# Optimization experiments

Measured on AMD Instinct MI355X. Metric: run time of the kernel, lower is better.

The kernel has to match this reference:

```python
import jax, jax.numpy as jnp
import numpy as np

DT = 0.001
TAU_SYN_INV = 200.0  # norse default 1/5e-3
TAU_MEM_INV = 100.0  # norse default 1/1e-2
V_TH = 0.4
ALPHA = 10.0  # SuperSpike surrogate slope


@jax.custom_vjp
def heaviside(x):
    # SuperSpike: heaviside forward, 1/(alpha*|x|+1)^2 surrogate backward
    return (x > 0).astype(x.dtype)

def _h_fwd(x):
    return heaviside(x), x

def _h_bwd(x, g):
    return (g / (ALPHA * jnp.abs(x) + 1.0) ** 2,)

heaviside.defvjp(_h_fwd, _h_bwd)


def conv(x, w, b, stride=1):
    y = jax.lax.conv_general_dilated(
        x, w, (stride, stride), 'VALID',
        dimension_numbers=('NCHW', 'OIHW', 'NCHW'))
    return y + b[None, :, None, None]


def maxpool2(x):
    return jax.lax.reduce_window(x, -jnp.inf, jax.lax.max, (1, 1, 2, 2), (1, 1, 2, 2), 'VALID')


def setup_inputs() -> dict:
    key = jax.random.key(0)
    ks = jax.random.split(key, 11)
    B, T, H, W = 32, 64, 64, 64
    num_classes = 10
    F = 96 * 12 * 12  # flattened encoder size = 13824
    HID = 128

    def u(k, shape, fan_in):
        bound = 1.0 / np.sqrt(fan_in)
        return jax.random.uniform(k, shape, jnp.float32, -bound, bound)

    return dict(
        x=jax.random.normal(ks[0], (B, T, 1, H, W), jnp.float32),
        w1=u(ks[1], (32, 1, 5, 5), 25), b1=u(ks[2], (32,), 25),
        w2=u(ks[3], (64, 32, 3, 3), 32 * 9), b2=u(ks[4], (64,), 32 * 9),
        w3=u(ks[5], (96, 64, 3, 3), 64 * 9), b3=u(ks[6], (96,), 64 * 9),
        w_in=jax.random.normal(ks[7], (HID, F), jnp.float32) / np.sqrt(F),
        w_rec=jax.random.normal(ks[8], (HID, HID), jnp.float32) / np.sqrt(HID),
        w_fc=u(ks[9], (num_classes, HID), HID),
        b_fc=u(ks[10], (num_classes,), HID),
    )


def reference(x, w1, b1, w2, b2, w3, b3, w_in, w_rec, w_fc, b_fc):
    B, T = x.shape[0], x.shape[1]
    HID = w_in.shape[0]
    C = w_fc.shape[0]

    # encoder vectorized over all B*T frames
    frames = x.reshape(B * T, x.shape[2], x.shape[3], x.shape[4])
    z = jax.nn.relu(conv(frames, w1, b1, stride=2))  # [BT,32,30,30]
    z = jax.nn.relu(conv(z, w2, b2))                 # [BT,64,28,28]
    z = maxpool2(z)                                  # [BT,64,14,14]
    z = jax.nn.relu(conv(z, w3, b3))                 # [BT,96,12,12]
    feats = z.reshape(B, T, -1)                      # [B,T,13824]

    # precompute feed-forward input currents for all timesteps
    ff = jnp.einsum('btf,hf->tbh', feats, w_in)      # [T,B,HID]

    def step(carry, ff_t):
        z_p, v, i, vr, ir = carry
        # LIF recurrent cell (norse lif_step, v_leak=0, v_reset=0)
        v_dec = v + DT * TAU_MEM_INV * (-v + i)
        i_dec = i - DT * TAU_SYN_INV * i
        z_n = heaviside(v_dec - V_TH)
        v_n = (1.0 - z_n) * v_dec
        i_n = i_dec + ff_t + z_p @ w_rec.T  # recurrent uses previous spikes
        # readout linear + LI cell (norse li_feed_forward_step)
        ro = z_n @ w_fc.T + b_fc
        vr_n = vr + DT * TAU_MEM_INV * (-vr + ir)
        ir_n = ir - DT * TAU_SYN_INV * ir + ro
        return (z_n, v_n, i_n, vr_n, ir_n), vr_n

    zeros_h = jnp.zeros((B, HID), x.dtype)
    zeros_c = jnp.zeros((B, C), x.dtype)
    carry0 = (zeros_h, zeros_h, zeros_h, zeros_c, zeros_c)
    _, voltages = jax.lax.scan(step, carry0, ff)     # [T,B,C]

    out = jnp.max(voltages, axis=0)                  # [B,C]
    return jax.nn.log_softmax(out, axis=1)
```

## Files before the change

### kernel.cpp

```cpp
#include <hip/hip_runtime.h>
#include <math.h>

typedef _Float16 half8 __attribute__((ext_vector_type(8)));
typedef _Float16 half4 __attribute__((ext_vector_type(4)));
typedef float f32x16 __attribute__((ext_vector_type(16)));

__global__ __launch_bounds__(256) void xprep_k(const float* __restrict__ x,
                                               _Float16* __restrict__ xh,
                                               _Float16* __restrict__ xl) {
  const int i = blockIdx.x * 256 + threadIdx.x;
  if (i >= 2097152) return;
  const float4 v = *(const float4*)(x + (size_t)i * 4);
  half4 h, l;
  const float vv[4] = {v.x, v.y, v.z, v.w};
#pragma unroll
  for (int e = 0; e < 4; ++e) {
    const _Float16 hh = (_Float16)vv[e];
    h[e] = hh;
    l[e] = (_Float16)((vv[e] - (float)hh) * 1024.0f);
  }
  *(half4*)(xh + (size_t)i * 4) = h;
  *(half4*)(xl + (size_t)i * 4) = l;
}

__global__ __launch_bounds__(256) void w1prep_k(const float* __restrict__ w1,
                                                _Float16* __restrict__ w1p) {
  const int i = blockIdx.x * 256 + threadIdx.x;
  if (i >= 1024) return;
  const int blk = i >> 8;
  const int s = blk >> 1, g = blk & 1;
  const int ch = (i >> 3) & 31, e = i & 7;
  const int k = s * 16 + g * 8 + e;
  float v = 0.f;
  if (k < 25) v = w1[ch * 25 + k];
  const _Float16 h = (_Float16)v;
  w1p[i] = h;
  w1p[1024 + i] = (_Float16)((v - (float)h) * 1024.0f);
}

__global__ __launch_bounds__(256) void w2prep_k(const float* __restrict__ w2,
                                                _Float16* __restrict__ w2p) {
  const int i = blockIdx.x * 256 + threadIdx.x;
  if (i >= 18432) return;
  const int tap = i >> 11;
  const int r = i & 2047;
  const int blk = r >> 8;
  const int nt = blk >> 2, s = (blk >> 1) & 1, g = blk & 1;
  const int n = (r >> 3) & 31, e = r & 7;
  const int och = nt * 32 + n;
  const int ic = s * 16 + g * 8 + e;
  const float v = w2[och * 288 + ic * 9 + tap];
  const _Float16 h = (_Float16)v;
  const _Float16 l = (_Float16)((v - (float)h) * 1024.0f);
  w2p[i] = h;
  w2p[18432 + i] = l;
}

__global__ __launch_bounds__(256) void w3prep_k(const float* __restrict__ w3,
                                                _Float16* __restrict__ w3p) {
  const int i = blockIdx.x * 256 + threadIdx.x;
  if (i >= 55296) return;
  const int icc = i / 27648;
  const int r1 = i - icc * 27648;
  const int tc = r1 / 6144;
  const int rem = r1 - tc * 6144;
  const int tl = rem / 3072;
  const int rem2 = rem - tl * 3072;
  const int nt = rem2 >> 10;
  const int s = (rem2 >> 9) & 1;
  const int g = (rem2 >> 8) & 1;
  const int n = (rem2 >> 3) & 31;
  const int e = rem2 & 7;
  const int tap = tc * 2 + tl;
  const int och = nt * 32 + n;
  const int ic = icc * 32 + s * 16 + g * 8 + e;
  const float v = w3[(size_t)och * 576 + ic * 9 + tap];
  const _Float16 h = (_Float16)v;
  const _Float16 l = (_Float16)((v - (float)h) * 1024.0f);
  w3p[i] = h;
  w3p[55296 + i] = l;
}

__global__ __launch_bounds__(256) void winprep_k(const float* __restrict__ w_in,
                                                 _Float16* __restrict__ winp) {
  const int i = blockIdx.x * 256 + threadIdx.x;
  if (i >= 1769472) return;
  const int ks = i >> 11;
  const int rem = i & 2047;
  const int nt = rem >> 9;
  const int g = (rem >> 8) & 1;
  const int n = (rem >> 3) & 31;
  const int e = rem & 7;
  const int h = nt * 32 + n;
  const int k = ks * 16 + g * 8 + e;
  const float v = w_in[(size_t)h * 13824 + k];
  const _Float16 hh = (_Float16)v;
  const _Float16 ll = (_Float16)((v - (float)hh) * 1024.0f);
  winp[i] = hh;
  winp[1769472 + i] = ll;
}

__global__ __launch_bounds__(448) void conv2f_mfma_k(
    const _Float16* __restrict__ xh, const _Float16* __restrict__ xl,
    const float* __restrict__ b1, const _Float16* __restrict__ w1p,
    const _Float16* __restrict__ w2p, const float* __restrict__ b2,
    _Float16* __restrict__ y2s) {
  __shared__ __align__(16) _Float16 S[31232];
  const int rp = blockIdx.x;
  const int img0 = blockIdx.y * 2;
  const int tid = threadIdx.x;

  const int w = tid >> 6;
  const int lane = tid & 63;
  const int l31 = lane & 31;
  const int g = lane >> 5;

  {
    const float b1c = b1[l31];
    const int gb = l31 >> 3, e0 = l31 & 7;
    int xoffs[16];
#pragma unroll
    for (int s = 0; s < 2; ++s)
#pragma unroll
      for (int e = 0; e < 8; ++e) {
        const int k = s * 16 + g * 8 + e;
        const int ky = k / 5, kx = k - (k / 5) * 5;
        xoffs[s * 8 + e] = (k < 25) ? (ky * 64 + kx) : -1;
      }
#pragma unroll 1
    for (int ph = 0; ph < 2; ++ph) {
      if (tid < 240) {
        const int plane = tid / 120;
        const int c8 = tid - plane * 120;
        const _Float16* src = (plane ? xl : xh) +
                              (size_t)(img0 + ph) * 4096 + rp * 512 + c8 * 8;
        *(float4*)&S[23040 + plane * 960 + c8 * 8] = *(const float4*)src;
      }
      __syncthreads();
      if (w < 6) {
        const int p = w * 32 + l31;
        const int pcl = (p < 180) ? p : 179;
        const int row = pcl / 30;
        const int col = pcl - row * 30;
        const int xb = (2 * row) * 64 + 2 * col;
        f32x16 acc_h = {}, acc_l = {};
#pragma unroll
        for (int s = 0; s < 2; ++s) {
          half8 ah, al;
#pragma unroll
          for (int e = 0; e < 8; ++e) {
            const int o = xoffs[s * 8 + e];
            _Float16 hv = (_Float16)0.f, lv = (_Float16)0.f;
            if (o >= 0) {
              hv = S[23040 + xb + o];
              lv = S[24000 + xb + o];
            }
            ah[e] = hv;
            al[e] = lv;
          }
          const _Float16* bp = w1p + ((s * 2 + g) * 32 + l31) * 8;
          half8 bh = *(const half8*)bp;
          half8 bl = *(const half8*)(bp + 1024);
          acc_h = __builtin_amdgcn_mfma_f32_32x32x16_f16(ah, bh, acc_h, 0, 0, 0);
          acc_l = __builtin_amdgcn_mfma_f32_32x32x16_f16(ah, bl, acc_l, 0, 0, 0);
          acc_l = __builtin_amdgcn_mfma_f32_32x32x16_f16(al, bh, acc_l, 0, 0, 0);
        }
#pragma unroll
        for (int r = 0; r < 16; ++r) {
          const int mrow = (r & 3) + 8 * (r >> 2) + 4 * g;
          const int pp = w * 32 + mrow;
          if (pp < 180) {
            const int cl = pp - (pp / 30) * 30;
            const int swz = (cl >> 1) & 3;
            const int addr = ph * 5760 + pp * 32 + ((gb ^ swz) << 3) + e0;
            const float val =
                fmaxf(acc_h[r] + acc_l[r] * 9.765625e-4f + b1c, 0.f);
            const _Float16 hh = (_Float16)val;
            S[addr] = hh;
            S[11520 + addr] = (_Float16)((val - (float)hh) * 1024.0f);
          }
        }
      }
      __syncthreads();
    }
  }

  const int m = w * 32 + l31;
  const int aimg = m / 112;
  const int apos = m - aimg * 112;
  const int ar = apos / 28;
  const int ax = apos - ar * 28;
  const int icg = g * 8;

  f32x16 acc00 = {}, acc01 = {}, acc10 = {}, acc11 = {};

#pragma unroll 1
  for (int tc = 0; tc < 5; ++tc) {
    __syncthreads();
    const int tap0 = tc * 2;
    const int ntaps = (tc == 4) ? 1 : 2;
    for (int c = tid; c < ntaps * 256; c += 448) {
      *(float4*)&S[23040 + c * 8] = *(const float4*)&w2p[tap0 * 2048 + c * 8];
      *(float4*)&S[27136 + c * 8] =
          *(const float4*)&w2p[18432 + tap0 * 2048 + c * 8];
    }
    __syncthreads();
#pragma unroll 1
    for (int tl = 0; tl < ntaps; ++tl) {
      const int tap = tap0 + tl;
      const int ky = tap / 3;
      const int kx = tap - ky * 3;
      const int acol = ax + kx;
      const int swzA = ((acol >> 1) & 3) << 3;
      const int abase = aimg * 5760 + ((ar + ky) * 30 + acol) * 32;
#pragma unroll
      for (int s = 0; s < 2; ++s) {
        const int icoA = (s * 16 + icg) ^ swzA;
        const int bo0 = 23040 + (((tl * 2 + 0) * 2 + s) * 2 + g) * 256 + l31 * 8;
        const int bo1 = 23040 + (((tl * 2 + 1) * 2 + s) * 2 + g) * 256 + l31 * 8;
        half8 ah = *(const half8*)&S[abase + icoA];
        half8 al = *(const half8*)&S[11520 + abase + icoA];
        half8 bh0 = *(const half8*)&S[bo0];
        half8 bl0 = *(const half8*)&S[bo0 + 4096];
        half8 bh1 = *(const half8*)&S[bo1];
        half8 bl1 = *(const half8*)&S[bo1 + 4096];
        acc00 = __builtin_amdgcn_mfma_f32_32x32x16_f16(ah, bh0, acc00, 0, 0, 0);
        acc10 = __builtin_amdgcn_mfma_f32_32x32x16_f16(ah, bl0, acc10, 0, 0, 0);
        acc10 = __builtin_amdgcn_mfma_f32_32x32x16_f16(al, bh0, acc10, 0, 0, 0);
        acc01 = __builtin_amdgcn_mfma_f32_32x32x16_f16(ah, bh1, acc01, 0, 0, 0);
        acc11 = __builtin_amdgcn_mfma_f32_32x32x16_f16(ah, bl1, acc11, 0, 0, 0);
        acc11 = __builtin_amdgcn_mfma_f32_32x32x16_f16(al, bh1, acc11, 0, 0, 0);
      }
    }
  }

  float* sPool = (float*)S;
#pragma unroll 1
  for (int ph = 0; ph < 2; ++ph) {
    __syncthreads();
#pragma unroll
    for (int r = 0; r < 16; ++r) {
      const int mrow = (r & 3) + 8 * (r >> 2) + 4 * g;
      const int mo = w * 32 + mrow;
      const int srow = mo - ph * 112;
      if (srow >= 0 && srow < 112) {
        sPool[srow * 68 + l31] = acc00[r] + acc10[r] * 9.765625e-4f;
        sPool[srow * 68 + 32 + l31] = acc01[r] + acc11[r] * 9.765625e-4f;
      }
    }
    __syncthreads();
    if (tid < 224) {
      const int pr = tid / 112;
      const int r2 = tid - pr * 112;
      const int pc = r2 >> 3;
      const int blk = r2 & 7;
      const int m00 = pr * 56 + pc * 2;
      const float* s0 = &sPool[m00 * 68 + blk * 8];
      float rowv[4][8];
      *(float4*)&rowv[0][0] = *(const float4*)s0;
      *(float4*)&rowv[0][4] = *(const float4*)(s0 + 4);
      *(float4*)&rowv[1][0] = *(const float4*)(s0 + 68);
      *(float4*)&rowv[1][4] = *(const float4*)(s0 + 72);
      *(float4*)&rowv[2][0] = *(const float4*)(s0 + 28 * 68);
      *(float4*)&rowv[2][4] = *(const float4*)(s0 + 28 * 68 + 4);
      *(float4*)&rowv[3][0] = *(const float4*)(s0 + 29 * 68);
      *(float4*)&rowv[3][4] = *(const float4*)(s0 + 29 * 68 + 4);
      half8 hv, lv;
#pragma unroll
      for (int e = 0; e < 8; ++e) {
        const float mx = fmaxf(fmaxf(rowv[0][e], rowv[1][e]),
                               fmaxf(rowv[2][e], rowv[3][e]));
        const float val = fmaxf(mx + b2[blk * 8 + e], 0.f);
        const _Float16 hh = (_Float16)val;
        hv[e] = hh;
        lv[e] = (_Float16)((val - (float)hh) * 1024.0f);
      }
      const int posg = (rp * 2 + pr) * 14 + pc;
      const int icc = blk >> 2;
      const int slot = (blk & 3) ^ ((posg >> 1) & 3);
      _Float16* dh = y2s + (size_t)(img0 + ph) * 25088 + icc * 6272 +
                     posg * 32 + slot * 8;
      *(float4*)dh = *(float4*)&hv;
      *(float4*)(dh + 12544) = *(float4*)&lv;
    }
  }
}

__global__ __launch_bounds__(320) void conv3_mfma_k(
    const _Float16* __restrict__ y2s, const _Float16* __restrict__ w3p,
    const float* __restrict__ b3, _Float16* __restrict__ fh,
    _Float16* __restrict__ fl) {
  __shared__ __align__(16) _Float16 S[12544];
  const int img = blockIdx.x;
  const int tid = threadIdx.x;
  const int w = tid >> 6;
  const int lane = tid & 63;
  const int l31 = lane & 31;
  const int g = lane >> 5;
  const int m = w * 32 + l31;
  const int mc = (m < 144) ? m : 143;
  const int r = mc / 12, c = mc - (mc / 12) * 12;

  f32x16 acch[3] = {};
  f32x16 accl[3] = {};

  const _Float16* bb = w3p + g * 256 + l31 * 8;
#pragma unroll 1
  for (int icc = 0; icc < 2; ++icc) {
    __syncthreads();
    {
      const _Float16* src = y2s + (size_t)img * 25088 + icc * 6272;
      for (int c8 = tid; c8 < 784; c8 += 320) {
        *(float4*)&S[c8 * 8] = *(const float4*)&src[c8 * 8];
        *(float4*)&S[6272 + c8 * 8] = *(const float4*)&src[12544 + c8 * 8];
      }
    }
    __syncthreads();
#pragma unroll 1
    for (int tc = 0; tc < 5; ++tc) {
      const int ntaps = (tc == 4) ? 1 : 2;
#pragma unroll 1
      for (int tl = 0; tl < ntaps; ++tl) {
        const int tap = tc * 2 + tl;
        const int ky = tap / 3, kx = tap - (tap / 3) * 3;
        const int pix = (r + ky) * 14 + (c + kx);
        const int pswz = (pix >> 1) & 3;
        half8 ah[2], al[2];
#pragma unroll
        for (int s = 0; s < 2; ++s) {
          const int o = pix * 32 + ((s * 2 + g) ^ pswz) * 8;
          ah[s] = *(const half8*)&S[o];
          al[s] = *(const half8*)&S[6272 + o];
        }
        const _Float16* bt = bb + icc * 27648 + tc * 6144 + tl * 3072;
#pragma unroll
        for (int nt = 0; nt < 3; ++nt) {
#pragma unroll
          for (int s = 0; s < 2; ++s) {
            const _Float16* bp = bt + nt * 1024 + s * 512;
            half8 bh = *(const half8*)bp;
            half8 bl = *(const half8*)(bp + 55296);
            acch[nt] =
                __builtin_amdgcn_mfma_f32_32x32x16_f16(ah[s], bh, acch[nt], 0, 0, 0);
            accl[nt] =
                __builtin_amdgcn_mfma_f32_32x32x16_f16(ah[s], bl, accl[nt], 0, 0, 0);
            accl[nt] =
                __builtin_amdgcn_mfma_f32_32x32x16_f16(al[s], bh, accl[nt], 0, 0, 0);
          }
        }
      }
    }
  }
  float* sO = (float*)S;
#pragma unroll
  for (int nt = 0; nt < 3; ++nt) {
    __syncthreads();
#pragma unroll
    for (int rr = 0; rr < 16; ++rr) {
      const int row = (rr & 3) + 8 * (rr >> 2) + 4 * g;
      const int pos = w * 32 + row;
      if (pos < 144)
        sO[l31 * 145 + pos] = acch[nt][rr] + accl[nt][rr] * 9.765625e-4f;
    }
    __syncthreads();
    for (int idx8 = tid; idx8 < 576; idx8 += 320) {
      const int oc = idx8 / 18;
      const int pb = idx8 - oc * 18;
      const float bb2 = b3[nt * 32 + oc];
      half8 hv, lv;
#pragma unroll
      for (int e = 0; e < 8; ++e) {
        const float v = fmaxf(sO[oc * 145 + pb * 8 + e] + bb2, 0.f);
        const _Float16 hh = (_Float16)v;
        hv[e] = hh;
        lv[e] = (_Float16)((v - (float)hh) * 1024.0f);
      }
      const size_t ko = (size_t)img * 13824 + (nt * 32 + oc) * 144 + pb * 8;
      *(float4*)&fh[ko] = *(float4*)&hv;
      *(float4*)&fl[ko] = *(float4*)&lv;
    }
  }
}

__global__ __launch_bounds__(256) void ffgemm_k(
    const _Float16* __restrict__ fh, const _Float16* __restrict__ fl,
    const _Float16* __restrict__ winp, float* __restrict__ P, int frame0,
    int Cl) {
  __shared__ __align__(16) _Float16 S[24576];
  const int mb = blockIdx.x;
  const int kc = blockIdx.y;
  const int tid = threadIdx.x;
  const int w = tid >> 6;
  const int lane = tid & 63;
  const int l31 = lane & 31;
  const int g = lane >> 5;
  const int mt = w >> 1;
  const int nt0 = (w & 1) * 2;
  f32x16 acc_h[2] = {};
  f32x16 acc_l[2] = {};
  const int kbase = kc * 1728;
#pragma unroll 1
  for (int kt = 0; kt < 27; ++kt) {
    __syncthreads();
    for (int i = tid; i < 512; i += 256) {
      const int row = i >> 3, kb = i & 7;
      int rc = mb * 64 + row;
      if (rc >= Cl) rc = Cl - 1;
      const size_t so = (size_t)rc * 13824 + kbase + kt * 64 + kb * 8;
      const int d = row * 64 + ((kb ^ (row & 7)) * 8);
      *(float4*)&S[d] = *(const float4*)&fh[so];
      *(float4*)&S[4096 + d] = *(const float4*)&fl[so];
    }
    {
      const size_t bo = (size_t)(kc * 108 + kt * 4) * 2048;
      for (int i = tid; i < 1024; i += 256) {
        *(float4*)&S[8192 + i * 8] = *(const float4*)&winp[bo + i * 8];
        *(float4*)&S[16384 + i * 8] =
            *(const float4*)&winp[1769472 + bo + i * 8];
      }
    }
    __syncthreads();
#pragma unroll
    for (int ks = 0; ks < 4; ++ks) {
      const int kb = ks * 2 + g;
      const int ao = (mt * 32 + l31) * 64 + ((kb ^ (l31 & 7)) * 8);
      half8 ah = *(const half8*)&S[ao];
      half8 al = *(const half8*)&S[4096 + ao];
#pragma unroll
      for (int j = 0; j < 2; ++j) {
        const int nt = nt0 + j;
        const int b = 8192 + (((ks * 4 + nt) * 2 + g) * 32 + l31) * 8;
        half8 bh = *(const half8*)&S[b];
        half8 bl = *(const half8*)&S[8192 + b];
        acc_h[j] = __builtin_amdgcn_mfma_f32_32x32x16_f16(ah, bh, acc_h[j], 0, 0, 0);
        acc_l[j] = __builtin_amdgcn_mfma_f32_32x32x16_f16(ah, bl, acc_l[j], 0, 0, 0);
        acc_l[j] = __builtin_amdgcn_mfma_f32_32x32x16_f16(al, bh, acc_l[j], 0, 0, 0);
      }
    }
  }
  float* Pp = P + ((size_t)kc * 2048 + (size_t)frame0) * 128;
#pragma unroll
  for (int j = 0; j < 2; ++j) {
    const int h = (nt0 + j) * 32 + l31;
#pragma unroll
    for (int r = 0; r < 16; ++r) {
      const int row = (r & 3) + 8 * (r >> 2) + 4 * g;
      const int fr = mb * 64 + mt * 32 + row;
      if (fr < Cl)
        Pp[(size_t)fr * 128 + h] = acc_h[j][r] + acc_l[j][r] * 9.765625e-4f;
    }
  }
}

__global__ __launch_bounds__(256) void ffreduce_k(const float* __restrict__ P,
                                                  float* __restrict__ ffo) {
  const int i = blockIdx.x * 256 + threadIdx.x;
  float s = 0.f;
#pragma unroll
  for (int kcc = 0; kcc < 8; ++kcc) s += P[(size_t)kcc * 262144 + i];
  ffo[i] = s;
}

__global__ __launch_bounds__(64) void scan_k(
    const float* __restrict__ ff, const float* __restrict__ w_rec,
    const float* __restrict__ w_fc, const float* __restrict__ b_fc,
    float* __restrict__ out) {
#pragma clang fp contract(off)
  __shared__ float sWr[16384];
  const int b = blockIdx.x;
  const int t = threadIdx.x;
  for (int idx = t; idx < 16384; idx += 64) {
    int hh = idx >> 7, j = idx & 127;
    sWr[j * 128 + hh] = w_rec[idx];
  }
  float wf0[10], wf1[10], bf[10];
#pragma unroll
  for (int c = 0; c < 10; ++c) {
    wf0[c] = w_fc[c * 128 + t];
    wf1[c] = w_fc[c * 128 + 64 + t];
    bf[c] = b_fc[c];
  }
  __syncthreads();
  float v0 = 0.f, v1 = 0.f, i0 = 0.f, i1 = 0.f;
  float vr[10], ir[10], vmax[10];
#pragma unroll
  for (int c = 0; c < 10; ++c) {
    vr[c] = 0.f;
    ir[c] = 0.f;
    vmax[c] = -1e30f;
  }
  unsigned long long pm0 = 0ull, pm1 = 0ull;
  const float* ffb = ff + (size_t)b * 8192;
#pragma unroll 1
  for (int ts = 0; ts < 64; ++ts) {
    const float vd0 = v0 + 0.1f * (i0 - v0);
    const float vd1 = v1 + 0.1f * (i1 - v1);
    const float id0 = i0 - 0.2f * i0;
    const float id1 = i1 - 0.2f * i1;
    const bool z0 = (vd0 - 0.4f) > 0.f;
    const bool z1 = (vd1 - 0.4f) > 0.f;
    v0 = z0 ? 0.f : vd0;
    v1 = z1 ? 0.f : vd1;
    float rec0 = 0.f, rec1 = 0.f;
    unsigned long long mm = pm0;
    while (mm) {
      int j = __ffsll(mm) - 1;
      mm &= mm - 1;
      rec0 += sWr[j * 128 + t];
      rec1 += sWr[j * 128 + t + 64];
    }
    mm = pm1;
    while (mm) {
      int j = __ffsll(mm) - 1;
      mm &= mm - 1;
      rec0 += sWr[(j + 64) * 128 + t];
      rec1 += sWr[(j + 64) * 128 + t + 64];
    }
    i0 = (id0 + ffb[ts * 128 + t]) + rec0;
    i1 = (id1 + ffb[ts * 128 + 64 + t]) + rec1;
    pm0 = __ballot(z0);
    pm1 = __ballot(z1);
#pragma unroll
    for (int c = 0; c < 10; ++c) {
      float val = (z0 ? wf0[c] : 0.f) + (z1 ? wf1[c] : 0.f);
      val += __shfl_xor(val, 1);
      val += __shfl_xor(val, 2);
      val += __shfl_xor(val, 4);
      val += __shfl_xor(val, 8);
      val += __shfl_xor(val, 16);
      val += __shfl_xor(val, 32);
      const float ro = val + bf[c];
      vr[c] = vr[c] + 0.1f * (ir[c] - vr[c]);
      vmax[c] = fmaxf(vmax[c], vr[c]);
      ir[c] = (ir[c] - 0.2f * ir[c]) + ro;
    }
  }
  if (t == 0) {
    float M = vmax[0];
#pragma unroll
    for (int c = 1; c < 10; ++c) M = fmaxf(M, vmax[c]);
    float s = 0.f;
#pragma unroll
    for (int c = 0; c < 10; ++c) s += expf(vmax[c] - M);
    const float ls = logf(s);
#pragma unroll
    for (int c = 0; c < 10; ++c) out[b * 10 + c] = vmax[c] - M - ls;
  }
}

extern "C" void kernel_launch(void* const* d_in, const int* in_sizes, int n_in,
                              void* d_out, int out_size, void* d_ws,
                              size_t ws_size, hipStream_t stream) {
  (void)in_sizes;
  (void)n_in;
  (void)out_size;
  const float* x = (const float*)d_in[0];
  const float* w1 = (const float*)d_in[1];
  const float* b1 = (const float*)d_in[2];
  const float* w2 = (const float*)d_in[3];
  const float* b2 = (const float*)d_in[4];
  const float* w3 = (const float*)d_in[5];
  const float* b3 = (const float*)d_in[6];
  const float* w_in = (const float*)d_in[7];
  const float* w_rec = (const float*)d_in[8];
  const float* w_fc = (const float*)d_in[9];
  const float* b_fc = (const float*)d_in[10];
  float* out = (float*)d_out;
  char* ws = (char*)d_ws;

  const size_t OFF_W2P = 1048576ull + 8388608ull;
  const size_t OFF_W3P = OFF_W2P + 147456ull;
  const size_t OFF_WIN = OFF_W3P + 221184ull;
  const size_t OFF_W1P = OFF_WIN + 7077888ull;
  const size_t OFF_XH = OFF_W1P + 8192ull;
  const size_t OFF_XL = OFF_XH + 16777216ull;
  const size_t HDR = OFF_XL + 16777216ull;
  const size_t PERF = 50176ull + 55296ull;
  int C = 32;
  for (int c = 2048; c >= 32; c >>= 1) {
    if (HDR + (size_t)c * PERF <= ws_size) { C = c; break; }
  }
  float* ffbuf = (float*)ws;
  float* P = (float*)(ws + 1048576ull);
  _Float16* w2p = (_Float16*)(ws + OFF_W2P);
  _Float16* w3p = (_Float16*)(ws + OFF_W3P);
  _Float16* winp = (_Float16*)(ws + OFF_WIN);
  _Float16* w1p = (_Float16*)(ws + OFF_W1P);
  _Float16* xh = (_Float16*)(ws + OFF_XH);
  _Float16* xl = (_Float16*)(ws + OFF_XL);
  _Float16* y2s = (_Float16*)(ws + HDR);
  _Float16* fh = (_Float16*)(ws + HDR + (size_t)C * 50176ull);
  _Float16* fl = fh + (size_t)C * 13824;

  xprep_k<<<8192, 256, 0, stream>>>(x, xh, xl);
  w1prep_k<<<4, 256, 0, stream>>>(w1, w1p);
  w2prep_k<<<72, 256, 0, stream>>>(w2, w2p);
  w3prep_k<<<216, 256, 0, stream>>>(w3, w3p);
  winprep_k<<<6912, 256, 0, stream>>>(w_in, winp);

  const int nChunks = 2048 / C;
  const int mbN = (C + 63) / 64;
  for (int ch = 0; ch < nChunks; ++ch) {
    const int f0 = ch * C;
    conv2f_mfma_k<<<dim3(7, C / 2), 448, 0, stream>>>(
        xh + (size_t)f0 * 4096, xl + (size_t)f0 * 4096, b1, w1p, w2p, b2, y2s);
    conv3_mfma_k<<<C, 320, 0, stream>>>(y2s, w3p, b3, fh, fl);
    ffgemm_k<<<dim3(mbN, 8), 256, 0, stream>>>(fh, fl, winp, P, f0, C);
  }
  ffreduce_k<<<1024, 256, 0, stream>>>(P, ffbuf);
  scan_k<<<32, 64, 0, stream>>>(ffbuf, w_rec, w_fc, b_fc, out);
}
```

Measured before the change: 592.7 us.

## Shrink ffgemm M-tile to 32 rows for more blocks per chunk

The feed-forward GEMM tile drops from 64 to 32 frame rows per block. Each of the four waves now owns one 32-wide hidden-unit slice instead of a 2x2 layout. This doubles the number of blocks per chunk and cuts shared memory and accumulator registers, aiming for better occupancy and CU coverage. In exchange, every block reloads the full w_in tile for only half as many rows, which doubles weight traffic and lowers data reuse.

```diff
diff --git a/kernel.cpp b/kernel.cpp
--- a/kernel.cpp
+++ b/kernel.cpp
@@ -386,7 +386,7 @@
     const _Float16* __restrict__ fh, const _Float16* __restrict__ fl,
     const _Float16* __restrict__ winp, float* __restrict__ P, int frame0,
     int Cl) {
-  __shared__ __align__(16) _Float16 S[24576];
+  __shared__ __align__(16) _Float16 S[20480];
   const int mb = blockIdx.x;
   const int kc = blockIdx.y;
   const int tid = threadIdx.x;
@@ -394,28 +394,26 @@
   const int lane = tid & 63;
   const int l31 = lane & 31;
   const int g = lane >> 5;
-  const int mt = w >> 1;
-  const int nt0 = (w & 1) * 2;
-  f32x16 acc_h[2] = {};
-  f32x16 acc_l[2] = {};
+  f32x16 acc_h = {};
+  f32x16 acc_l = {};
   const int kbase = kc * 1728;
 #pragma unroll 1
   for (int kt = 0; kt < 27; ++kt) {
     __syncthreads();
-    for (int i = tid; i < 512; i += 256) {
-      const int row = i >> 3, kb = i & 7;
-      int rc = mb * 64 + row;
+    {
+      const int row = tid >> 3, kb = tid & 7;
+      int rc = mb * 32 + row;
       if (rc >= Cl) rc = Cl - 1;
       const size_t so = (size_t)rc * 13824 + kbase + kt * 64 + kb * 8;
       const int d = row * 64 + ((kb ^ (row & 7)) * 8);
       *(float4*)&S[d] = *(const float4*)&fh[so];
-      *(float4*)&S[4096 + d] = *(const float4*)&fl[so];
+      *(float4*)&S[2048 + d] = *(const float4*)&fl[so];
     }
     {
       const size_t bo = (size_t)(kc * 108 + kt * 4) * 2048;
       for (int i = tid; i < 1024; i += 256) {
-        *(float4*)&S[8192 + i * 8] = *(const float4*)&winp[bo + i * 8];
-        *(float4*)&S[16384 + i * 8] =
+        *(float4*)&S[4096 + i * 8] = *(const float4*)&winp[bo + i * 8];
+        *(float4*)&S[12288 + i * 8] =
             *(const float4*)&winp[1769472 + bo + i * 8];
       }
     }
@@ -423,32 +421,24 @@
 #pragma unroll
     for (int ks = 0; ks < 4; ++ks) {
       const int kb = ks * 2 + g;
-      const int ao = (mt * 32 + l31) * 64 + ((kb ^ (l31 & 7)) * 8);
+      const int ao = l31 * 64 + ((kb ^ (l31 & 7)) * 8);
       half8 ah = *(const half8*)&S[ao];
-      half8 al = *(const half8*)&S[4096 + ao];
-#pragma unroll
-      for (int j = 0; j < 2; ++j) {
-        const int nt = nt0 + j;
-        const int b = 8192 + (((ks * 4 + nt) * 2 + g) * 32 + l31) * 8;
-        half8 bh = *(const half8*)&S[b];
-        half8 bl = *(const half8*)&S[8192 + b];
-        acc_h[j] = __builtin_amdgcn_mfma_f32_32x32x16_f16(ah, bh, acc_h[j], 0, 0, 0);
-        acc_l[j] = __builtin_amdgcn_mfma_f32_32x32x16_f16(ah, bl, acc_l[j], 0, 0, 0);
-        acc_l[j] = __builtin_amdgcn_mfma_f32_32x32x16_f16(al, bh, acc_l[j], 0, 0, 0);
-      }
+      half8 al = *(const half8*)&S[2048 + ao];
+      const int b = 4096 + (((ks * 4 + w) * 2 + g) * 32 + l31) * 8;
+      half8 bh = *(const half8*)&S[b];
+      half8 bl = *(const half8*)&S[b + 8192];
+      acc_h = __builtin_amdgcn_mfma_f32_32x32x16_f16(ah, bh, acc_h, 0, 0, 0);
+      acc_l = __builtin_amdgcn_mfma_f32_32x32x16_f16(ah, bl, acc_l, 0, 0, 0);
+      acc_l = __builtin_amdgcn_mfma_f32_32x32x16_f16(al, bh, acc_l, 0, 0, 0);
     }
   }
   float* Pp = P + ((size_t)kc * 2048 + (size_t)frame0) * 128;
-#pragma unroll
-  for (int j = 0; j < 2; ++j) {
-    const int h = (nt0 + j) * 32 + l31;
-#pragma unroll
-    for (int r = 0; r < 16; ++r) {
-      const int row = (r & 3) + 8 * (r >> 2) + 4 * g;
-      const int fr = mb * 64 + mt * 32 + row;
-      if (fr < Cl)
-        Pp[(size_t)fr * 128 + h] = acc_h[j][r] + acc_l[j][r] * 9.765625e-4f;
-    }
+  const int h = w * 32 + l31;
+#pragma unroll
+  for (int r = 0; r < 16; ++r) {
+    const int row = (r & 3) + 8 * (r >> 2) + 4 * g;
+    const int fr = mb * 32 + row;
+    if (fr < Cl) Pp[(size_t)fr * 128 + h] = acc_h[r] + acc_l[r] * 9.765625e-4f;
   }
 }
 
@@ -599,7 +589,7 @@
   winprep_k<<<6912, 256, 0, stream>>>(w_in, winp);
 
   const int nChunks = 2048 / C;
-  const int mbN = (C + 63) / 64;
+  const int mbN = (C + 31) / 32;
   for (int ch = 0; ch < nChunks; ++ch) {
     const int f0 = ch * C;
     conv2f_mfma_k<<<dim3(7, C / 2), 448, 0, stream>>>(
```

New measurement: 578.4 us. -2.4%, faster.
